# Kernel optimization log

Hardware: AMD Instinct MI355X
Metric: run time of the kernel (lower is better)

Reference implementation:

```python
import jax, jax.numpy as jnp
import numpy as np

B, S, D, H = 2, 2048, 1024, 16
HD = D // H  # per-head dim = 64


def setup_inputs() -> dict:
    key = jax.random.key(0)
    ks = jax.random.split(key, 9)
    s = 0.02
    return {
        "h": jax.random.normal(ks[0], (B, S, D), jnp.float32),
        "Wq": jax.random.normal(ks[1], (D, D), jnp.float32) * s,
        "bq": jax.random.normal(ks[2], (D,), jnp.float32) * s,
        "Wk": jax.random.normal(ks[3], (D, D), jnp.float32) * s,
        "bk": jax.random.normal(ks[4], (D,), jnp.float32) * s,
        "Wv": jax.random.normal(ks[5], (D, D), jnp.float32) * s,
        "bv": jax.random.normal(ks[6], (D,), jnp.float32) * s,
        "Wo": jax.random.normal(ks[7], (D, D), jnp.float32) * s,
        "bo": jax.random.normal(ks[8], (D,), jnp.float32) * s,
    }


def reference(h, Wq, bq, Wk, bk, Wv, bv, Wo, bo):
    b, s, d = h.shape
    # Linear projections (torch Linear: x @ W.T + b), split heads -> [B,H,S,HD]
    def split_heads(x):
        return x.reshape(b, s, H, HD).transpose(0, 2, 1, 3)

    q = split_heads(h @ Wq.T + bq)
    k = split_heads(h @ Wk.T + bk)
    v = split_heads(h @ Wv.T + bv)

    # scaled scores [B,H,S,S]
    qk = jnp.einsum("bhqd,bhkd->bhqk", q, k) / np.sqrt(HD).astype(np.float32)
    # causal mask: strictly upper triangle -> -inf
    causal = jnp.triu(jnp.ones((s, s), dtype=bool), k=1)
    qk = jnp.where(causal[None, None], -jnp.inf, qk)

    probs = jax.nn.softmax(qk, axis=-1)
    o = jnp.einsum("bhqk,bhkd->bhqd", probs, v)
    o = o.transpose(0, 2, 1, 3).reshape(b, s, d)
    return o @ Wo.T + bo
```

## Files before the change

kernel.cpp:

```cpp
#include <hip/hip_runtime.h>
#include <stdint.h>

typedef __bf16 bf16;
typedef __bf16 bf16x4_t __attribute__((ext_vector_type(4)));
typedef __bf16 bf16x8_t __attribute__((ext_vector_type(8)));
typedef float f32x4 __attribute__((ext_vector_type(4)));

static constexpr int NB = 2, SS = 2048, DD = 1024, NH = 16, HD = 64;

__device__ __forceinline__ void gl_lds16(const void* g, void* l) {
    __builtin_amdgcn_global_load_lds((__attribute__((address_space(1))) void*)g,
                                     (__attribute__((address_space(3))) void*)l, 16, 0, 0);
}

__global__ __launch_bounds__(256) void cast_all(const float* __restrict__ h,
                                                const float* __restrict__ Wq,
                                                const float* __restrict__ Wk,
                                                const float* __restrict__ Wv,
                                                const float* __restrict__ Wo,
                                                bf16* __restrict__ dst) {
    int i = blockIdx.x * 256 + threadIdx.x;
    const float* src;
    int off;
    if (i < 1048576) { src = h; off = i; }
    else {
        int r = i - 1048576;
        int w = r >> 18;
        off = r & 262143;
        src = (w == 0) ? Wq : (w == 1) ? Wk : (w == 2) ? Wv : Wo;
    }
    float4 v = reinterpret_cast<const float4*>(src)[off];
    bf16x4_t o;
    o.x = (bf16)v.x; o.y = (bf16)v.y; o.z = (bf16)v.z; o.w = (bf16)v.w;
    reinterpret_cast<bf16x4_t*>(dst)[i] = o;
}

__device__ __forceinline__ void gemm128_mainloop(const bf16* __restrict__ Ablk,
                                                 const bf16* __restrict__ Bblk,
                                                 int K, f32x4 acc[4][4]) {
    __shared__ __align__(16) bf16 As[128 * 32];
    __shared__ __align__(16) bf16 Bs[128 * 32];
    const int tid = threadIdx.x;
    const int wave = tid >> 6, lane = tid & 63;
    const int quad = lane >> 4, l15 = lane & 15;
    const int wm = wave >> 1, wn = wave & 1;

#pragma unroll
    for (int mi = 0; mi < 4; mi++)
#pragma unroll
        for (int ni = 0; ni < 4; ni++) {
            acc[mi][ni][0] = 0.f; acc[mi][ni][1] = 0.f;
            acc[mi][ni][2] = 0.f; acc[mi][ni][3] = 0.f;
        }

    const int n0c = tid;
    const int r0 = n0c >> 2, c0 = (n0c & 3) ^ ((r0 >> 1) & 3);
    const int n1c = 256 + tid;
    const int r1 = n1c >> 2, c1 = (n1c & 3) ^ ((r1 >> 1) & 3);

    for (int kk = 0; kk < K; kk += 32) {
        __syncthreads();
        gl_lds16(Ablk + (size_t)r0 * K + kk + c0 * 8, &As[(wave * 64) * 8]);
        gl_lds16(Ablk + (size_t)r1 * K + kk + c1 * 8, &As[(256 + wave * 64) * 8]);
        gl_lds16(Bblk + (size_t)r0 * K + kk + c0 * 8, &Bs[(wave * 64) * 8]);
        gl_lds16(Bblk + (size_t)r1 * K + kk + c1 * 8, &Bs[(256 + wave * 64) * 8]);
        __syncthreads();

        bf16x8_t a[4], b[4];
#pragma unroll
        for (int mi = 0; mi < 4; mi++) {
            int R = wm * 64 + mi * 16 + l15;
            a[mi] = *(const bf16x8_t*)&As[R * 32 + ((quad ^ ((R >> 1) & 3)) << 3)];
        }
#pragma unroll
        for (int ni = 0; ni < 4; ni++) {
            int R = wn * 64 + ni * 16 + l15;
            b[ni] = *(const bf16x8_t*)&Bs[R * 32 + ((quad ^ ((R >> 1) & 3)) << 3)];
        }
#pragma unroll
        for (int mi = 0; mi < 4; mi++)
#pragma unroll
            for (int ni = 0; ni < 4; ni++)
                acc[mi][ni] = __builtin_amdgcn_mfma_f32_16x16x32_bf16(a[mi], b[ni], acc[mi][ni], 0, 0, 0);
    }
}

__global__ __launch_bounds__(256) void gemm_qkv(const bf16* __restrict__ A, const bf16* __restrict__ Wqkv,
                                                const float* __restrict__ bq, const float* __restrict__ bk,
                                                const float* __restrict__ bv,
                                                bf16* __restrict__ Qb, bf16* __restrict__ Kb, bf16* __restrict__ Vb) {
    const int m0 = blockIdx.x * 128;
    const int n0 = blockIdx.y * 128;
    f32x4 acc[4][4];
    gemm128_mainloop(A + (size_t)m0 * DD, Wqkv + (size_t)n0 * DD, DD, acc);

    const int tid = threadIdx.x, wave = tid >> 6, lane = tid & 63;
    const int quad = lane >> 4, l15 = lane & 15;
    const int wm = wave >> 1, wn = wave & 1;

    const int which = n0 >> 10;
    const float* bias = (which == 0) ? bq : (which == 1) ? bk : bv;
    bf16* dst = (which == 0) ? Qb : (which == 1) ? Kb : Vb;
    const float sc = (which == 0) ? 0.18033688f : 1.0f;

    const int cbase = (n0 & 1023) + wn * 64;
    const int head = cbase >> 6;
    const int bb = m0 >> 11;
    const int s0 = (m0 & 2047) + wm * 64;
    bf16* dbase = dst + ((size_t)(bb * NH + head)) * SS * HD;

#pragma unroll
    for (int ni = 0; ni < 4; ni++) {
        float bsv = bias[cbase + ni * 16 + l15];
        int hd = ni * 16 + l15;
#pragma unroll
        for (int mi = 0; mi < 4; mi++) {
#pragma unroll
            for (int r = 0; r < 4; r++) {
                int s = s0 + mi * 16 + quad * 4 + r;
                dbase[(size_t)s * HD + hd] = (bf16)((acc[mi][ni][r] + bsv) * sc);
            }
        }
    }
}

__global__ __launch_bounds__(256) void gemm_out(const bf16* __restrict__ A, const bf16* __restrict__ Wo,
                                                const float* __restrict__ bo, float* __restrict__ out) {
    const int m0 = blockIdx.x * 128, n0 = blockIdx.y * 128;
    f32x4 acc[4][4];
    gemm128_mainloop(A + (size_t)m0 * DD, Wo + (size_t)n0 * DD, DD, acc);

    const int tid = threadIdx.x, wave = tid >> 6, lane = tid & 63;
    const int quad = lane >> 4, l15 = lane & 15;
    const int wm = wave >> 1, wn = wave & 1;
    float* obase = out + (size_t)(m0 + wm * 64) * DD + n0 + wn * 64;
#pragma unroll
    for (int ni = 0; ni < 4; ni++) {
        float bias = bo[n0 + wn * 64 + ni * 16 + l15];
#pragma unroll
        for (int mi = 0; mi < 4; mi++)
#pragma unroll
            for (int r = 0; r < 4; r++)
                obase[(size_t)(mi * 16 + quad * 4 + r) * DD + ni * 16 + l15] = acc[mi][ni][r] + bias;
    }
}

__global__ __launch_bounds__(256, 3) void attn_kernel(const bf16* __restrict__ Qb, const bf16* __restrict__ Kb,
                                                      const bf16* __restrict__ Vb, bf16* __restrict__ Ob) {
    __shared__ __align__(16) bf16 Kt[128 * 64];
    __shared__ __align__(16) bf16 Vt[64 * 136];
    __shared__ __align__(16) bf16 Pt[4 * 32 * 64];

    const int tid = threadIdx.x, wave = tid >> 6, lane = tid & 63;
    const int quad = lane >> 4, l15 = lane & 15;
    const int bx = blockIdx.x;
    const int ii = bx >> 5, bh = bx & 31;
    const int qtile = (ii < 8) ? (15 - ii) : (ii - 8);
    const size_t hoff = (size_t)bh * SS * HD;
    const bf16* Qg = Qb + hoff + (size_t)qtile * 128 * HD;

    bf16x8_t qf[2][2];
#pragma unroll
    for (int qt = 0; qt < 2; qt++)
#pragma unroll
        for (int ks = 0; ks < 2; ks++)
            qf[qt][ks] = *(const bf16x8_t*)(Qg + (wave * 32 + qt * 16 + l15) * HD + ks * 32 + quad * 8);

    f32x4 o[2][4];
#pragma unroll
    for (int qt = 0; qt < 2; qt++)
#pragma unroll
        for (int nO = 0; nO < 4; nO++) {
            o[qt][nO][0] = 0.f; o[qt][nO][1] = 0.f; o[qt][nO][2] = 0.f; o[qt][nO][3] = 0.f;
        }
    float mrow[2] = {-__builtin_inff(), -__builtin_inff()};
    float lrow[2] = {0.f, 0.f};

    bf16* Pw = &Pt[wave * 2048];

    for (int j = 0; j <= qtile; j++) {
        __syncthreads();
        const bf16* Kg = Kb + hoff + (size_t)j * 128 * HD;
#pragma unroll
        for (int t = 0; t < 4; t++) {
            int n = t * 256 + tid;
            int row = n >> 3, gc = (n & 7) ^ (row & 7);
            gl_lds16(Kg + row * HD + gc * 8, &Kt[(t * 256 + wave * 64) * 8]);
        }
        const bf16* Vg = Vb + hoff + (size_t)j * 128 * HD;
        {
            int k0 = (tid & 31) * 4, d0 = (tid >> 5) * 8;
            bf16x8_t v0 = *(const bf16x8_t*)(Vg + (k0 + 0) * HD + d0);
            bf16x8_t v1 = *(const bf16x8_t*)(Vg + (k0 + 1) * HD + d0);
            bf16x8_t v2 = *(const bf16x8_t*)(Vg + (k0 + 2) * HD + d0);
            bf16x8_t v3 = *(const bf16x8_t*)(Vg + (k0 + 3) * HD + d0);
#pragma unroll
            for (int jj = 0; jj < 8; jj++) {
                bf16x4_t w;
                w.x = v0[jj]; w.y = v1[jj]; w.z = v2[jj]; w.w = v3[jj];
                *(bf16x4_t*)&Vt[(d0 + jj) * 136 + k0] = w;
            }
        }
        __syncthreads();

        const bool diag = (j == qtile);
#pragma unroll 1
        for (int kh = 0; kh < 2; kh++) {
            if (diag && kh == 1 && wave < 2) break;

            f32x4 st[4][2];
#pragma unroll
            for (int kt = 0; kt < 4; kt++)
#pragma unroll
                for (int qt = 0; qt < 2; qt++) {
                    st[kt][qt][0] = 0.f; st[kt][qt][1] = 0.f; st[kt][qt][2] = 0.f; st[kt][qt][3] = 0.f;
                }
#pragma unroll
            for (int ks = 0; ks < 2; ks++) {
#pragma unroll
                for (int kt = 0; kt < 4; kt++) {
                    int R = (kh * 4 + kt) * 16 + l15;
                    bf16x8_t kf = *(const bf16x8_t*)&Kt[R * HD + ((((ks << 2) | quad) ^ (R & 7)) << 3)];
#pragma unroll
                    for (int qt = 0; qt < 2; qt++)
                        st[kt][qt] = __builtin_amdgcn_mfma_f32_16x16x32_bf16(kf, qf[qt][ks], st[kt][qt], 0, 0, 0);
                }
            }
            if (diag) {
#pragma unroll
                for (int kt = 0; kt < 4; kt++)
#pragma unroll
                    for (int qt = 0; qt < 2; qt++)
#pragma unroll
                        for (int r = 0; r < 4; r++) {
                            int key = kh * 64 + kt * 16 + quad * 4 + r;
                            int row = wave * 32 + qt * 16 + l15;
                            if (key > row) st[kt][qt][r] = -__builtin_inff();
                        }
            }

#pragma unroll
            for (int qt = 0; qt < 2; qt++) {
                float mx = -__builtin_inff();
#pragma unroll
                for (int kt = 0; kt < 4; kt++)
#pragma unroll
                    for (int r = 0; r < 4; r++) mx = fmaxf(mx, st[kt][qt][r]);
                mx = fmaxf(mx, __shfl_xor(mx, 16));
                mx = fmaxf(mx, __shfl_xor(mx, 32));
                float mnew = fmaxf(mrow[qt], mx);
                float alpha = exp2f(mrow[qt] - mnew);
                mrow[qt] = mnew;
                float sum = 0.f;
                const int row = qt * 16 + l15;
#pragma unroll
                for (int kt = 0; kt < 4; kt++) {
                    float p0 = exp2f(st[kt][qt][0] - mnew);
                    float p1 = exp2f(st[kt][qt][1] - mnew);
                    float p2 = exp2f(st[kt][qt][2] - mnew);
                    float p3 = exp2f(st[kt][qt][3] - mnew);
                    sum += (p0 + p1) + (p2 + p3);
                    bf16x4_t pb;
                    pb.x = (bf16)p0; pb.y = (bf16)p1; pb.z = (bf16)p2; pb.w = (bf16)p3;
                    int c = kt * 2 + (quad >> 1);
                    *(bf16x4_t*)&Pw[row * 64 + ((c ^ (row & 7)) << 3) + ((quad & 1) << 2)] = pb;
                }
                sum += __shfl_xor(sum, 16);
                sum += __shfl_xor(sum, 32);
                lrow[qt] = lrow[qt] * alpha + sum;
#pragma unroll
                for (int r = 0; r < 4; r++) {
                    float a = __shfl(alpha, (lane & 48) | (quad * 4 + r));
#pragma unroll
                    for (int nO = 0; nO < 4; nO++) o[qt][nO][r] *= a;
                }
            }

#pragma unroll
            for (int ks = 0; ks < 2; ks++) {
                bf16x8_t pf[2];
#pragma unroll
                for (int qt = 0; qt < 2; qt++) {
                    int row = qt * 16 + l15;
                    int c = (ks << 2) | quad;
                    pf[qt] = *(const bf16x8_t*)&Pw[row * 64 + ((c ^ (row & 7)) << 3)];
                }
#pragma unroll
                for (int nO = 0; nO < 4; nO++) {
                    bf16x8_t vf = *(const bf16x8_t*)&Vt[(nO * 16 + l15) * 136 + kh * 64 + ks * 32 + quad * 8];
#pragma unroll
                    for (int qt = 0; qt < 2; qt++)
                        o[qt][nO] = __builtin_amdgcn_mfma_f32_16x16x32_bf16(pf[qt], vf, o[qt][nO], 0, 0, 0);
                }
            }
        }
    }

    const int bb = bh >> 4, hh = bh & 15;
#pragma unroll
    for (int qt = 0; qt < 2; qt++) {
#pragma unroll
        for (int r = 0; r < 4; r++) {
            float linv = 1.f / __shfl(lrow[qt], (lane & 48) | (quad * 4 + r));
            int srow = qtile * 128 + wave * 32 + qt * 16 + quad * 4 + r;
#pragma unroll
            for (int nO = 0; nO < 4; nO++)
                Ob[((size_t)(bb * SS + srow)) * DD + hh * HD + nO * 16 + l15] = (bf16)(o[qt][nO][r] * linv);
        }
    }
}

extern "C" void kernel_launch(void* const* d_in, const int* in_sizes, int n_in,
                              void* d_out, int out_size, void* d_ws, size_t ws_size,
                              hipStream_t stream) {
    (void)in_sizes; (void)n_in; (void)out_size; (void)ws_size;
    const float* h  = (const float*)d_in[0];
    const float* Wq = (const float*)d_in[1];
    const float* bq = (const float*)d_in[2];
    const float* Wk = (const float*)d_in[3];
    const float* bk = (const float*)d_in[4];
    const float* Wv = (const float*)d_in[5];
    const float* bv = (const float*)d_in[6];
    const float* Wo = (const float*)d_in[7];
    const float* bo = (const float*)d_in[8];
    float* out = (float*)d_out;

    char* ws = (char*)d_ws;
    bf16* hbf  = (bf16*)(ws);
    bf16* wqkv = (bf16*)(ws + 8388608);
    bf16* wo   = (bf16*)(ws + 8388608 + 6291456);
    bf16* Qb   = (bf16*)(ws + 16777216);
    bf16* Kb   = (bf16*)(ws + 16777216 + 8388608);
    bf16* Vb   = (bf16*)(ws + 16777216 + 2 * 8388608);
    bf16* Ob   = (bf16*)(ws + 16777216 + 3 * 8388608);

    cast_all<<<8192, 256, 0, stream>>>(h, Wq, Wk, Wv, Wo, hbf);
    gemm_qkv<<<dim3(32, 24), 256, 0, stream>>>(hbf, wqkv, bq, bk, bv, Qb, Kb, Vb);
    attn_kernel<<<512, 256, 0, stream>>>(Qb, Kb, Vb, Ob);
    gemm_out<<<dim3(32, 8), 256, 0, stream>>>(Ob, wo, bo, out);
}
```

Measured before the change: 205.7 us.

## Split long causal attention tiles across blocks with a merge pass; shrink output GEMM tile

Query tiles 8–15 are now split into two KV-range parts using a static schedule table, so the attention grid grows from 512 to 768 blocks of roughly equal work. Each split part writes unnormalized partial outputs in bf16 plus row max and row sum to scratch, and a new merge kernel combines the two parts with log-sum-exp weights. The aim is to fix the load imbalance that causal masking creates, where the longest query tiles dominate runtime. The output projection also switches to 64x128 tiles, doubling its block count to fill the CUs better. In exchange it adds an extra launch, scratch traffic, and some bf16 rounding of unnormalized partials.

```diff
diff --git a/kernel.cpp b/kernel.cpp
--- a/kernel.cpp
+++ b/kernel.cpp
@@ -85,6 +85,55 @@
     }
 }
 
+__device__ __forceinline__ void gemm64_mainloop(const bf16* __restrict__ Ablk,
+                                                const bf16* __restrict__ Bblk,
+                                                int K, f32x4 acc[2][4]) {
+    __shared__ __align__(16) bf16 As[64 * 32];
+    __shared__ __align__(16) bf16 Bs[128 * 32];
+    const int tid = threadIdx.x;
+    const int wave = tid >> 6, lane = tid & 63;
+    const int quad = lane >> 4, l15 = lane & 15;
+    const int wm = wave >> 1, wn = wave & 1;
+
+#pragma unroll
+    for (int mi = 0; mi < 2; mi++)
+#pragma unroll
+        for (int ni = 0; ni < 4; ni++) {
+            acc[mi][ni][0] = 0.f; acc[mi][ni][1] = 0.f;
+            acc[mi][ni][2] = 0.f; acc[mi][ni][3] = 0.f;
+        }
+
+    const int ra = tid >> 2, ca = (tid & 3) ^ ((ra >> 1) & 3);
+    const int r0 = tid >> 2, c0 = (tid & 3) ^ ((r0 >> 1) & 3);
+    const int n1c = 256 + tid;
+    const int r1 = n1c >> 2, c1 = (n1c & 3) ^ ((r1 >> 1) & 3);
+
+    for (int kk = 0; kk < K; kk += 32) {
+        __syncthreads();
+        gl_lds16(Ablk + (size_t)ra * K + kk + ca * 8, &As[(wave * 64) * 8]);
+        gl_lds16(Bblk + (size_t)r0 * K + kk + c0 * 8, &Bs[(wave * 64) * 8]);
+        gl_lds16(Bblk + (size_t)r1 * K + kk + c1 * 8, &Bs[(256 + wave * 64) * 8]);
+        __syncthreads();
+
+        bf16x8_t a[2], b[4];
+#pragma unroll
+        for (int mi = 0; mi < 2; mi++) {
+            int R = wm * 32 + mi * 16 + l15;
+            a[mi] = *(const bf16x8_t*)&As[R * 32 + ((quad ^ ((R >> 1) & 3)) << 3)];
+        }
+#pragma unroll
+        for (int ni = 0; ni < 4; ni++) {
+            int R = wn * 64 + ni * 16 + l15;
+            b[ni] = *(const bf16x8_t*)&Bs[R * 32 + ((quad ^ ((R >> 1) & 3)) << 3)];
+        }
+#pragma unroll
+        for (int mi = 0; mi < 2; mi++)
+#pragma unroll
+            for (int ni = 0; ni < 4; ni++)
+                acc[mi][ni] = __builtin_amdgcn_mfma_f32_16x16x32_bf16(a[mi], b[ni], acc[mi][ni], 0, 0, 0);
+    }
+}
+
 __global__ __launch_bounds__(256) void gemm_qkv(const bf16* __restrict__ A, const bf16* __restrict__ Wqkv,
                                                 const float* __restrict__ bq, const float* __restrict__ bk,
                                                 const float* __restrict__ bv,
@@ -126,19 +175,19 @@
 
 __global__ __launch_bounds__(256) void gemm_out(const bf16* __restrict__ A, const bf16* __restrict__ Wo,
                                                 const float* __restrict__ bo, float* __restrict__ out) {
-    const int m0 = blockIdx.x * 128, n0 = blockIdx.y * 128;
-    f32x4 acc[4][4];
-    gemm128_mainloop(A + (size_t)m0 * DD, Wo + (size_t)n0 * DD, DD, acc);
+    const int m0 = blockIdx.x * 64, n0 = blockIdx.y * 128;
+    f32x4 acc[2][4];
+    gemm64_mainloop(A + (size_t)m0 * DD, Wo + (size_t)n0 * DD, DD, acc);
 
     const int tid = threadIdx.x, wave = tid >> 6, lane = tid & 63;
     const int quad = lane >> 4, l15 = lane & 15;
     const int wm = wave >> 1, wn = wave & 1;
-    float* obase = out + (size_t)(m0 + wm * 64) * DD + n0 + wn * 64;
+    float* obase = out + (size_t)(m0 + wm * 32) * DD + n0 + wn * 64;
 #pragma unroll
     for (int ni = 0; ni < 4; ni++) {
         float bias = bo[n0 + wn * 64 + ni * 16 + l15];
 #pragma unroll
-        for (int mi = 0; mi < 4; mi++)
+        for (int mi = 0; mi < 2; mi++)
 #pragma unroll
             for (int r = 0; r < 4; r++)
                 obase[(size_t)(mi * 16 + quad * 4 + r) * DD + ni * 16 + l15] = acc[mi][ni][r] + bias;
@@ -146,7 +195,12 @@
 }
 
 __global__ __launch_bounds__(256, 3) void attn_kernel(const bf16* __restrict__ Qb, const bf16* __restrict__ Kb,
-                                                      const bf16* __restrict__ Vb, bf16* __restrict__ Ob) {
+                                                      const bf16* __restrict__ Vb, bf16* __restrict__ Ob,
+                                                      bf16* __restrict__ Opart, float* __restrict__ Ml) {
+    constexpr int PQ[24]  = {15,15,14, 7,14,13,13,12, 6,12,11,11,10, 5,10, 9, 9, 8, 4, 8, 3, 2, 1, 0};
+    constexpr int PJ0[24] = { 0, 8, 0, 0, 8, 0, 7, 0, 0, 7, 0, 6, 0, 0, 6, 0, 5, 0, 0, 5, 0, 0, 0, 0};
+    constexpr int PJ1[24] = { 8,16, 8, 8,15, 7,14, 7, 7,13, 6,12, 6, 6,11, 5,10, 5, 5, 9, 4, 3, 2, 1};
+
     __shared__ __align__(16) bf16 Kt[128 * 64];
     __shared__ __align__(16) bf16 Vt[64 * 136];
     __shared__ __align__(16) bf16 Pt[4 * 32 * 64];
@@ -154,8 +208,9 @@
     const int tid = threadIdx.x, wave = tid >> 6, lane = tid & 63;
     const int quad = lane >> 4, l15 = lane & 15;
     const int bx = blockIdx.x;
-    const int ii = bx >> 5, bh = bx & 31;
-    const int qtile = (ii < 8) ? (15 - ii) : (ii - 8);
+    const int p = bx >> 5, bh = bx & 31;
+    const int qtile = PQ[p], jbeg = PJ0[p], jend = PJ1[p];
+    const bool diagpart = (jend == qtile + 1);
     const size_t hoff = (size_t)bh * SS * HD;
     const bf16* Qg = Qb + hoff + (size_t)qtile * 128 * HD;
 
@@ -178,7 +233,7 @@
 
     bf16* Pw = &Pt[wave * 2048];
 
-    for (int j = 0; j <= qtile; j++) {
+    for (int j = jbeg; j < jend; j++) {
         __syncthreads();
         const bf16* Kg = Kb + hoff + (size_t)j * 128 * HD;
 #pragma unroll
@@ -203,7 +258,7 @@
         }
         __syncthreads();
 
-        const bool diag = (j == qtile);
+        const bool diag = diagpart && (j == jend - 1);
 #pragma unroll 1
         for (int kh = 0; kh < 2; kh++) {
             if (diag && kh == 1 && wave < 2) break;
@@ -296,17 +351,66 @@
         }
     }
 
+    if (qtile >= 8) {
+        const int pidx = ((bh << 3) + (qtile - 8)) * 2 + (jbeg != 0 ? 1 : 0);
+        bf16* Op = Opart + (size_t)pidx * (128 * 64);
+        float* mlp = Ml + (size_t)pidx * 256;
+#pragma unroll
+        for (int qt = 0; qt < 2; qt++) {
+            if (quad == 0) {
+                mlp[wave * 32 + qt * 16 + l15] = mrow[qt];
+                mlp[128 + wave * 32 + qt * 16 + l15] = lrow[qt];
+            }
+#pragma unroll
+            for (int r = 0; r < 4; r++) {
+                int row = wave * 32 + qt * 16 + quad * 4 + r;
+#pragma unroll
+                for (int nO = 0; nO < 4; nO++)
+                    Op[row * 64 + nO * 16 + l15] = (bf16)o[qt][nO][r];
+            }
+        }
+    } else {
+        const int bb = bh >> 4, hh = bh & 15;
+#pragma unroll
+        for (int qt = 0; qt < 2; qt++) {
+#pragma unroll
+            for (int r = 0; r < 4; r++) {
+                float linv = 1.f / __shfl(lrow[qt], (lane & 48) | (quad * 4 + r));
+                int srow = qtile * 128 + wave * 32 + qt * 16 + quad * 4 + r;
+#pragma unroll
+                for (int nO = 0; nO < 4; nO++)
+                    Ob[((size_t)(bb * SS + srow)) * DD + hh * HD + nO * 16 + l15] = (bf16)(o[qt][nO][r] * linv);
+            }
+        }
+    }
+}
+
+__global__ __launch_bounds__(256) void merge_kernel(const bf16* __restrict__ Opart,
+                                                    const float* __restrict__ Ml,
+                                                    bf16* __restrict__ Ob) {
+    const int bh = blockIdx.x >> 3, q8 = blockIdx.x & 7;
+    const int p0 = ((bh << 3) + q8) * 2, p1 = p0 + 1;
+    const int t = threadIdx.x, row = t >> 1, c0 = (t & 1) * 32;
+    float m0 = Ml[p0 * 256 + row], l0 = Ml[p0 * 256 + 128 + row];
+    float m1 = Ml[p1 * 256 + row], l1 = Ml[p1 * 256 + 128 + row];
+    float M = fmaxf(m0, m1);
+    float w0 = exp2f(m0 - M), w1 = exp2f(m1 - M);
+    float inv = 1.f / (l0 * w0 + l1 * w1);
+    w0 *= inv; w1 *= inv;
+    const bf16* O0 = Opart + (size_t)p0 * (128 * 64) + row * 64 + c0;
+    const bf16* O1 = Opart + (size_t)p1 * (128 * 64) + row * 64 + c0;
     const int bb = bh >> 4, hh = bh & 15;
-#pragma unroll
-    for (int qt = 0; qt < 2; qt++) {
-#pragma unroll
-        for (int r = 0; r < 4; r++) {
-            float linv = 1.f / __shfl(lrow[qt], (lane & 48) | (quad * 4 + r));
-            int srow = qtile * 128 + wave * 32 + qt * 16 + quad * 4 + r;
-#pragma unroll
-            for (int nO = 0; nO < 4; nO++)
-                Ob[((size_t)(bb * SS + srow)) * DD + hh * HD + nO * 16 + l15] = (bf16)(o[qt][nO][r] * linv);
-        }
+    const int srow = (8 + q8) * 128 + row;
+    bf16* dst = Ob + ((size_t)(bb * SS + srow)) * DD + hh * HD + c0;
+#pragma unroll
+    for (int i = 0; i < 4; i++) {
+        bf16x8_t a = *(const bf16x8_t*)(O0 + i * 8);
+        bf16x8_t b = *(const bf16x8_t*)(O1 + i * 8);
+        bf16x8_t r;
+#pragma unroll
+        for (int jj = 0; jj < 8; jj++)
+            r[jj] = (bf16)((float)a[jj] * w0 + (float)b[jj] * w1);
+        *(bf16x8_t*)(dst + i * 8) = r;
     }
 }
 
@@ -333,9 +437,12 @@
     bf16* Kb   = (bf16*)(ws + 16777216 + 8388608);
     bf16* Vb   = (bf16*)(ws + 16777216 + 2 * 8388608);
     bf16* Ob   = (bf16*)(ws + 16777216 + 3 * 8388608);
+    bf16*  Opart = (bf16*)(ws);
+    float* Ml    = (float*)(ws + 8388608);
 
     cast_all<<<8192, 256, 0, stream>>>(h, Wq, Wk, Wv, Wo, hbf);
     gemm_qkv<<<dim3(32, 24), 256, 0, stream>>>(hbf, wqkv, bq, bk, bv, Qb, Kb, Vb);
-    attn_kernel<<<512, 256, 0, stream>>>(Qb, Kb, Vb, Ob);
-    gemm_out<<<dim3(32, 8), 256, 0, stream>>>(Ob, wo, bo, out);
-}
+    attn_kernel<<<768, 256, 0, stream>>>(Qb, Kb, Vb, Ob, Opart, Ml);
+    merge_kernel<<<256, 256, 0, stream>>>(Opart, Ml, Ob);
+    gemm_out<<<dim3(64, 8), 256, 0, stream>>>(Ob, wo, bo, out);
+}
```

Result: faster. 191.8 us (-6.7%).
